# Kernel tuning notes

Measured on AMD Instinct MI355X. Metric: run time of the kernel, lower is better.

## Reference

```python
import jax, jax.numpy as jnp
import numpy as np

N, E, D_IN, HID, H = 50000, 800000, 128, 64, 2
C = HID  # per-head dim (out_channels)


def _lin_params(key, fan_in, fan_out):
    kw, kb = jax.random.split(key)
    s = 1.0 / np.sqrt(fan_in)
    W = jax.random.uniform(kw, (fan_in, fan_out), jnp.float32, -s, s)
    b = jax.random.uniform(kb, (fan_out,), jnp.float32, -s, s)
    return W, b


def setup_inputs() -> dict:
    key = jax.random.key(0)
    ks = jax.random.split(key, 14)
    x = jax.random.normal(ks[0], (N, D_IN), jnp.float32)
    edge_index = jax.random.randint(ks[1], (2, E), 0, N, jnp.int32)
    inp = {"x": x, "edge_index": edge_index}
    dims = [D_IN, HID, HID]
    i = 2
    for L, d_in in enumerate(dims, start=1):
        for nm, fo in (("q", H * C), ("k", H * C), ("v", H * C), ("s", HID)):
            W, b = _lin_params(ks[i], d_in, fo)
            inp[f"W{L}{nm}"] = W
            inp[f"b{L}{nm}"] = b
            i += 1
            if i >= 14:
                ks = jax.random.split(ks[-1], 14)
                i = 0
    return inp


def _transformer_conv(x, src, dst, Wq, bq, Wk, bk, Wv, bv, Ws, bs):
    # x: [N, d_in] -> out: [N, HID]
    q = (x @ Wq + bq).reshape(N, H, C)
    k = (x @ Wk + bk).reshape(N, H, C)
    v = (x @ Wv + bv).reshape(N, H, C)
    qi = q[dst]                      # [E, H, C] gather at destination (query)
    kj = k[src]                      # [E, H, C] gather at source (key)
    alpha = jnp.sum(qi * kj, axis=-1) / jnp.sqrt(jnp.float32(C))  # [E, H]
    amax = jax.ops.segment_max(alpha, dst, num_segments=N)        # [N, H]
    ex = jnp.exp(alpha - amax[dst])                               # [E, H]
    denom = jax.ops.segment_sum(ex, dst, num_segments=N)          # [N, H]
    attn = ex / (denom[dst] + 1e-16)                              # [E, H]
    msg = v[src] * attn[:, :, None]                               # [E, H, C]
    out = jax.ops.segment_sum(msg, dst, num_segments=N)           # [N, H, C]
    out = out.mean(axis=1)                                        # concat=False: head mean
    return out + x @ Ws + bs                                      # root skip


def reference(x, edge_index,
              W1q, b1q, W1k, b1k, W1v, b1v, W1s, b1s,
              W2q, b2q, W2k, b2k, W2v, b2v, W2s, b2s,
              W3q, b3q, W3k, b3k, W3v, b3v, W3s, b3s):
    src, dst = edge_index[0], edge_index[1]
    h = jax.nn.relu(_transformer_conv(x, src, dst, W1q, b1q, W1k, b1k, W1v, b1v, W1s, b1s))
    h = jax.nn.relu(_transformer_conv(h, src, dst, W2q, b2q, W2k, b2k, W2v, b2v, W2s, b2s))
    h = jax.nn.relu(_transformer_conv(h, src, dst, W3q, b3q, W3k, b3k, W3v, b3v, W3s, b3s))
    return h
```

## Files before the change

### kernel.cpp

```cpp
#include <hip/hip_runtime.h>
#include <cstdint>

typedef _Float16 f16;
typedef __attribute__((ext_vector_type(2))) _Float16 f16x2;
typedef __attribute__((ext_vector_type(8))) _Float16 f16x8;
typedef __attribute__((ext_vector_type(4))) float f32x4;

#if defined(__has_builtin)
# if __has_builtin(__builtin_amdgcn_fdot2)
#  define HAVE_FDOT2 1
# endif
#endif


__global__ void hist_kernel(const int* __restrict__ dst, int* __restrict__ cnt, int E) {
    int e = blockIdx.x * blockDim.x + threadIdx.x;
    if (e < E) atomicAdd(&cnt[dst[e]], 1);
}

__global__ __launch_bounds__(256) void block_scan_kernel(
    const int* __restrict__ cnt, int* __restrict__ rowptr,
    int* __restrict__ partials, int n) {
    __shared__ int lds[256];
    int tid = threadIdx.x;
    int i = blockIdx.x * 256 + tid;
    int v = (i < n) ? cnt[i] : 0;
    lds[tid] = v;
    __syncthreads();
    for (int off = 1; off < 256; off <<= 1) {
        int t = (tid >= off) ? lds[tid - off] : 0;
        __syncthreads();
        lds[tid] += t;
        __syncthreads();
    }
    if (i < n) rowptr[i + 1] = lds[tid];
    if (tid == 255) partials[blockIdx.x] = lds[255];
}

__global__ __launch_bounds__(256) void partial_scan_kernel(int* __restrict__ partials, int nb) {
    __shared__ int lds[256];
    int tid = threadIdx.x;
    int v = (tid < nb) ? partials[tid] : 0;
    lds[tid] = v;
    __syncthreads();
    for (int off = 1; off < 256; off <<= 1) {
        int t = (tid >= off) ? lds[tid - off] : 0;
        __syncthreads();
        lds[tid] += t;
        __syncthreads();
    }
    if (tid < nb) partials[tid] = lds[tid] - v;
}

__global__ __launch_bounds__(256) void add_offsets_kernel(
    int* __restrict__ rowptr, const int* __restrict__ partials, int n) {
    int i = blockIdx.x * 256 + threadIdx.x;
    if (i < n) rowptr[i + 1] += partials[blockIdx.x];
    if (i == 0) rowptr[0] = 0;
}

__global__ void scatter_kernel(const int* __restrict__ src, const int* __restrict__ dst,
                               const int* __restrict__ rowptr, int* __restrict__ cnt,
                               int* __restrict__ src_sorted, int E) {
    int e = blockIdx.x * blockDim.x + threadIdx.x;
    if (e < E) {
        int d = dst[e];
        int p = rowptr[d] + atomicAdd(&cnt[d], 1);
        src_sorted[p] = src[e];
    }
}


__global__ __launch_bounds__(256) void prep_w_kernel(
    const float* __restrict__ Wq, const float* __restrict__ Wk,
    const float* __restrict__ Wv, const float* __restrict__ Ws,
    const float* __restrict__ bq, const float* __restrict__ bk,
    const float* __restrict__ bv, const float* __restrict__ bs,
    f16* __restrict__ Wf, float* __restrict__ bias, int K) {
    int idx = blockIdx.x * 256 + threadIdx.x;
    if (idx < 448) {
        bias[idx] = (idx < 128) ? bq[idx]
                  : (idx < 256) ? bk[idx - 128]
                  : (idx < 384) ? bv[idx - 256]
                  : bs[idx - 384];
    }
    if (idx >= 448 * K) return;
    int c = idx / K, k = idx - c * K;
    float v;
    if (c < 128)      v = Wq[k * 128 + c];
    else if (c < 256) v = Wk[k * 128 + (c - 128)];
    else if (c < 384) v = Wv[k * 128 + (c - 256)];
    else              v = Ws[k * 64 + (c - 384)];
    int NK = K >> 5;
    int ct = c >> 6, cf = (c >> 4) & 3, fr = c & 15;
    int ks = k >> 5, fk = (k >> 3) & 3, j = k & 7;
    size_t off = ((size_t)(((ct * 4 + cf) * NK + ks) * 4 + fk) * 16 + fr) * 8 + j;
    Wf[off] = (f16)v;
}


template <int K, bool F32IN>
__global__ __launch_bounds__(256) void gemm_qkvs_kernel(
    const void* __restrict__ Xv, const f16* __restrict__ Wf,
    const float* __restrict__ bias, f16* __restrict__ out, int M) {
    constexpr int NK = K / 32;
    int tid = threadIdx.x;
    int lane = tid & 63, wid = tid >> 6;
    int fr = lane & 15, fk = lane >> 4;
    int arow = blockIdx.x * 64 + wid * 16 + fr;
    int crow = (arow < M) ? arow : (M - 1);

    f16x8 af[NK];
    if (F32IN) {
        const float* X = (const float*)Xv + (size_t)crow * K;
        #pragma unroll
        for (int ks = 0; ks < NK; ++ks) {
            float4 lo = *(const float4*)(X + ks * 32 + fk * 8);
            float4 hi = *(const float4*)(X + ks * 32 + fk * 8 + 4);
            af[ks] = {(f16)lo.x, (f16)lo.y, (f16)lo.z, (f16)lo.w,
                      (f16)hi.x, (f16)hi.y, (f16)hi.z, (f16)hi.w};
        }
    } else {
        const f16* X = (const f16*)Xv + (size_t)crow * K;
        #pragma unroll
        for (int ks = 0; ks < NK; ++ks)
            af[ks] = *(const f16x8*)(X + ks * 32 + fk * 8);
    }

    int orow0 = blockIdx.x * 64 + wid * 16 + fk * 4;
    for (int ct = 0; ct < 7; ++ct) {
        f32x4 acc[4] = {};
        #pragma unroll
        for (int cf = 0; cf < 4; ++cf) {
            const f16* Wp = Wf + (size_t)(ct * 4 + cf) * NK * 512 + (size_t)lane * 8;
            #pragma unroll
            for (int ks = 0; ks < NK; ++ks) {
                f16x8 bf = *(const f16x8*)(Wp + (size_t)ks * 512);
                acc[cf] = __builtin_amdgcn_mfma_f32_16x16x32_f16(af[ks], bf, acc[cf], 0, 0, 0);
            }
        }
        int ocol = ct * 64 + fr;
        #pragma unroll
        for (int cf = 0; cf < 4; ++cf) {
            float b = bias[ocol + cf * 16];
            #pragma unroll
            for (int r = 0; r < 4; ++r) {
                int gr = orow0 + r;
                if (gr < M) out[(size_t)gr * 448 + ocol + cf * 16] = (f16)(acc[cf][r] + b);
            }
        }
    }
}


__global__ __launch_bounds__(256) void attn_kernel(
    const f16* __restrict__ T,
    const int* __restrict__ rowptr, const int* __restrict__ srcs,
    f16* __restrict__ hout, float* __restrict__ fout, int n, int final_layer) {
    int node = blockIdx.x * 4 + (threadIdx.x >> 6);
    if (node >= n) return;
    int lane = threadIdx.x & 63;
    int c8 = lane & 7, eg = lane >> 3;
    const size_t base = (size_t)node * 448;
    const int co = c8 * 8;

    f16x8 q0 = *(const f16x8*)(T + base + co);
    f16x8 q1 = *(const f16x8*)(T + base + 64 + co);
    float m0 = -__builtin_inff(), m1 = -__builtin_inff();
    float s0 = 0.f, s1 = 0.f;
    float av0[8] = {}, av1[8] = {};

    int beg = rowptr[node], end = rowptr[node + 1];
    if (beg < end) {
        int nsrc = srcs[min(beg + eg, end - 1)];
        for (int i0 = beg; i0 < end; i0 += 8) {
            int i = i0 + eg;
            bool valid = (i < end);
            int sidx = nsrc;
            if (i0 + 8 < end) nsrc = srcs[min(i + 8, end - 1)];

            const f16* p = T + (size_t)sidx * 448 + co;
            f16x8 k0 = *(const f16x8*)(p + 128);
            f16x8 k1 = *(const f16x8*)(p + 192);
            f16x8 v0 = *(const f16x8*)(p + 256);
            f16x8 v1 = *(const f16x8*)(p + 320);

            float d0 = 0.f, d1 = 0.f;
#ifdef HAVE_FDOT2
            #pragma unroll
            for (int j = 0; j < 4; ++j) {
                f16x2 a0 = {q0[2 * j], q0[2 * j + 1]};
                f16x2 b0 = {k0[2 * j], k0[2 * j + 1]};
                d0 = __builtin_amdgcn_fdot2(a0, b0, d0, false);
                f16x2 a1 = {q1[2 * j], q1[2 * j + 1]};
                f16x2 b1 = {k1[2 * j], k1[2 * j + 1]};
                d1 = __builtin_amdgcn_fdot2(a1, b1, d1, false);
            }
#else
            #pragma unroll
            for (int j = 0; j < 8; ++j) {
                d0 += (float)q0[j] * (float)k0[j];
                d1 += (float)q1[j] * (float)k1[j];
            }
#endif
            d0 += __shfl_xor(d0, 1); d1 += __shfl_xor(d1, 1);
            d0 += __shfl_xor(d0, 2); d1 += __shfl_xor(d1, 2);
            d0 += __shfl_xor(d0, 4); d1 += __shfl_xor(d1, 4);
            d0 *= 0.125f; d1 *= 0.125f;
            if (!valid) { d0 = -__builtin_inff(); d1 = -__builtin_inff(); }

            if (__any(d0 > m0 + 6.f || d1 > m1 + 6.f)) {
                float t0 = d0, t1 = d1;
                t0 = fmaxf(t0, __shfl_xor(t0, 8));  t1 = fmaxf(t1, __shfl_xor(t1, 8));
                t0 = fmaxf(t0, __shfl_xor(t0, 16)); t1 = fmaxf(t1, __shfl_xor(t1, 16));
                t0 = fmaxf(t0, __shfl_xor(t0, 32)); t1 = fmaxf(t1, __shfl_xor(t1, 32));
                float nm0 = fmaxf(m0, t0), nm1 = fmaxf(m1, t1);
                float f0 = __expf(m0 - nm0), f1 = __expf(m1 - nm1);
                s0 *= f0; s1 *= f1;
                #pragma unroll
                for (int j = 0; j < 8; ++j) { av0[j] *= f0; av1[j] *= f1; }
                m0 = nm0; m1 = nm1;
            }
            float p0 = __expf(d0 - m0);
            float p1 = __expf(d1 - m1);
            s0 += p0; s1 += p1;
            #pragma unroll
            for (int j = 0; j < 8; ++j) {
                av0[j] += p0 * (float)v0[j];
                av1[j] += p1 * (float)v1[j];
            }
        }
    }

    s0 += __shfl_xor(s0, 8);  s1 += __shfl_xor(s1, 8);
    s0 += __shfl_xor(s0, 16); s1 += __shfl_xor(s1, 16);
    s0 += __shfl_xor(s0, 32); s1 += __shfl_xor(s1, 32);
    float inv0 = 1.0f / (s0 + 1e-16f), inv1 = 1.0f / (s1 + 1e-16f);
    float r[8];
    #pragma unroll
    for (int j = 0; j < 8; ++j) {
        float a0 = av0[j], a1 = av1[j];
        a0 += __shfl_xor(a0, 8);  a1 += __shfl_xor(a1, 8);
        a0 += __shfl_xor(a0, 16); a1 += __shfl_xor(a1, 16);
        a0 += __shfl_xor(a0, 32); a1 += __shfl_xor(a1, 32);
        r[j] = 0.5f * (a0 * inv0 + a1 * inv1);
    }

    if (lane < 8) {
        f16x8 sk = *(const f16x8*)(T + base + 384 + co);
        #pragma unroll
        for (int j = 0; j < 8; ++j) r[j] = fmaxf(r[j] + (float)sk[j], 0.f);
        if (final_layer) {
            float4* dst4 = (float4*)(fout + (size_t)node * 64 + co);
            dst4[0] = make_float4(r[0], r[1], r[2], r[3]);
            dst4[1] = make_float4(r[4], r[5], r[6], r[7]);
        } else {
            f16x8 o = {(f16)r[0], (f16)r[1], (f16)r[2], (f16)r[3],
                       (f16)r[4], (f16)r[5], (f16)r[6], (f16)r[7]};
            *(f16x8*)(hout + (size_t)node * 64 + co) = o;
        }
    }
}


extern "C" void kernel_launch(void* const* d_in, const int* in_sizes, int n_in,
                              void* d_out, int out_size, void* d_ws, size_t ws_size,
                              hipStream_t stream) {
    const float* x = (const float*)d_in[0];
    const int* ei  = (const int*)d_in[1];
    const int N = in_sizes[0] / 128;
    const int E = in_sizes[1] / 2;
    const int* src = ei;
    const int* dst = ei + E;

    const float* Wq[3] = {(const float*)d_in[2],  (const float*)d_in[10], (const float*)d_in[18]};
    const float* bq[3] = {(const float*)d_in[3],  (const float*)d_in[11], (const float*)d_in[19]};
    const float* Wk[3] = {(const float*)d_in[4],  (const float*)d_in[12], (const float*)d_in[20]};
    const float* bk[3] = {(const float*)d_in[5],  (const float*)d_in[13], (const float*)d_in[21]};
    const float* Wv[3] = {(const float*)d_in[6],  (const float*)d_in[14], (const float*)d_in[22]};
    const float* bv[3] = {(const float*)d_in[7],  (const float*)d_in[15], (const float*)d_in[23]};
    const float* Wsk[3]= {(const float*)d_in[8],  (const float*)d_in[16], (const float*)d_in[24]};
    const float* bsk[3]= {(const float*)d_in[9],  (const float*)d_in[17], (const float*)d_in[25]};

    char* p = (char*)d_ws;
    int* rowptr   = (int*)p; p += (size_t)(N + 1) * 4;
    int* cnt      = (int*)p; p += (size_t)N * 4;
    int* srcs     = (int*)p; p += (size_t)E * 4;
    int* partials = (int*)p; p += 256 * 4;
    p = (char*)(((uintptr_t)p + 255) & ~(uintptr_t)255);
    f16* Xh   = (f16*)p; p += (size_t)N * 64 * 2;
    f16* QKVS = (f16*)p; p += (size_t)N * 448 * 2;
    f16* Wt0  = (f16*)p; p += (size_t)448 * 128 * 2;
    f16* Wt1  = (f16*)p; p += (size_t)448 * 64 * 2;
    f16* Wt2  = (f16*)p; p += (size_t)448 * 64 * 2;
    float* bias0 = (float*)p; p += 448 * 4;
    float* bias1 = (float*)p; p += 448 * 4;
    float* bias2 = (float*)p; p += 448 * 4;
    if ((size_t)(p - (char*)d_ws) > ws_size) return;

    f16* Wt[3] = {Wt0, Wt1, Wt2};
    float* bias[3] = {bias0, bias1, bias2};

    for (int l = 0; l < 3; ++l) {
        int K = (l == 0) ? 128 : 64;
        prep_w_kernel<<<(448 * K + 255) / 256, 256, 0, stream>>>(
            Wq[l], Wk[l], Wv[l], Wsk[l], bq[l], bk[l], bv[l], bsk[l], Wt[l], bias[l], K);
    }

    int nb = (N + 255) / 256;
    hipMemsetAsync(cnt, 0, (size_t)N * 4, stream);
    hist_kernel<<<(E + 255) / 256, 256, 0, stream>>>(dst, cnt, E);
    block_scan_kernel<<<nb, 256, 0, stream>>>(cnt, rowptr, partials, N);
    partial_scan_kernel<<<1, 256, 0, stream>>>(partials, nb);
    add_offsets_kernel<<<nb, 256, 0, stream>>>(rowptr, partials, N);
    hipMemsetAsync(cnt, 0, (size_t)N * 4, stream);
    scatter_kernel<<<(E + 255) / 256, 256, 0, stream>>>(src, dst, rowptr, cnt, srcs, E);

    int gx = (N + 63) / 64;
    for (int l = 0; l < 3; ++l) {
        if (l == 0)
            gemm_qkvs_kernel<128, true><<<gx, 256, 0, stream>>>(x, Wt[l], bias[l], QKVS, N);
        else
            gemm_qkvs_kernel<64, false><<<gx, 256, 0, stream>>>(Xh, Wt[l], bias[l], QKVS, N);
        attn_kernel<<<(N + 3) / 4, 256, 0, stream>>>(
            QKVS, rowptr, srcs, Xh, (float*)d_out, N, (l == 2) ? 1 : 0);
    }
}
```

Before: 358.6 us.

## Merge weight-prep launches, fold count reset into scan, prefetch K/V, shrink attn blocks

```diff
diff --git a/kernel.cpp b/kernel.cpp
--- a/kernel.cpp
+++ b/kernel.cpp
@@ -19,7 +19,7 @@
 }
 
 __global__ __launch_bounds__(256) void block_scan_kernel(
-    const int* __restrict__ cnt, int* __restrict__ rowptr,
+    int* __restrict__ cnt, int* __restrict__ rowptr,
     int* __restrict__ partials, int n) {
     __shared__ int lds[256];
     int tid = threadIdx.x;
@@ -33,7 +33,7 @@
         lds[tid] += t;
         __syncthreads();
     }
-    if (i < n) rowptr[i + 1] = lds[tid];
+    if (i < n) { rowptr[i + 1] = lds[tid]; cnt[i] = 0; }
     if (tid == 255) partials[blockIdx.x] = lds[255];
 }
 
@@ -71,31 +71,35 @@
 }
 
 
-__global__ __launch_bounds__(256) void prep_w_kernel(
-    const float* __restrict__ Wq, const float* __restrict__ Wk,
-    const float* __restrict__ Wv, const float* __restrict__ Ws,
-    const float* __restrict__ bq, const float* __restrict__ bk,
-    const float* __restrict__ bv, const float* __restrict__ bs,
-    f16* __restrict__ Wf, float* __restrict__ bias, int K) {
+struct PrepArgs {
+    const float* Wq[3]; const float* Wk[3]; const float* Wv[3]; const float* Ws[3];
+    const float* bq[3]; const float* bk[3]; const float* bv[3]; const float* bs[3];
+    f16* Wf[3]; float* bias[3];
+};
+
+__global__ __launch_bounds__(256) void prep_w_all_kernel(PrepArgs a) {
     int idx = blockIdx.x * 256 + threadIdx.x;
-    if (idx < 448) {
-        bias[idx] = (idx < 128) ? bq[idx]
-                  : (idx < 256) ? bk[idx - 128]
-                  : (idx < 384) ? bv[idx - 256]
-                  : bs[idx - 384];
-    }
-    if (idx >= 448 * K) return;
-    int c = idx / K, k = idx - c * K;
+    int l, loc, K;
+    if (idx < 448 * 128)      { l = 0; loc = idx;              K = 128; }
+    else if (idx < 448 * 192) { l = 1; loc = idx - 448 * 128;  K = 64;  }
+    else                      { l = 2; loc = idx - 448 * 192;  K = 64;  }
+    if (loc < 448) {
+        a.bias[l][loc] = (loc < 128) ? a.bq[l][loc]
+                       : (loc < 256) ? a.bk[l][loc - 128]
+                       : (loc < 384) ? a.bv[l][loc - 256]
+                       : a.bs[l][loc - 384];
+    }
+    int c = loc / K, k = loc - c * K;
     float v;
-    if (c < 128)      v = Wq[k * 128 + c];
-    else if (c < 256) v = Wk[k * 128 + (c - 128)];
-    else if (c < 384) v = Wv[k * 128 + (c - 256)];
-    else              v = Ws[k * 64 + (c - 384)];
+    if (c < 128)      v = a.Wq[l][k * 128 + c];
+    else if (c < 256) v = a.Wk[l][k * 128 + (c - 128)];
+    else if (c < 384) v = a.Wv[l][k * 128 + (c - 256)];
+    else              v = a.Ws[l][k * 64 + (c - 384)];
     int NK = K >> 5;
     int ct = c >> 6, cf = (c >> 4) & 3, fr = c & 15;
     int ks = k >> 5, fk = (k >> 3) & 3, j = k & 7;
     size_t off = ((size_t)(((ct * 4 + cf) * NK + ks) * 4 + fk) * 16 + fr) * 8 + j;
-    Wf[off] = (f16)v;
+    a.Wf[l][off] = (f16)v;
 }
 
 
@@ -153,11 +157,11 @@
 }
 
 
-__global__ __launch_bounds__(256) void attn_kernel(
+__global__ __launch_bounds__(128) void attn_kernel(
     const f16* __restrict__ T,
     const int* __restrict__ rowptr, const int* __restrict__ srcs,
     f16* __restrict__ hout, float* __restrict__ fout, int n, int final_layer) {
-    int node = blockIdx.x * 4 + (threadIdx.x >> 6);
+    int node = blockIdx.x * 2 + (threadIdx.x >> 6);
     if (node >= n) return;
     int lane = threadIdx.x & 63;
     int c8 = lane & 7, eg = lane >> 3;
@@ -172,62 +176,78 @@
 
     int beg = rowptr[node], end = rowptr[node + 1];
     if (beg < end) {
-        int nsrc = srcs[min(beg + eg, end - 1)];
-        for (int i0 = beg; i0 < end; i0 += 8) {
-            int i = i0 + eg;
-            bool valid = (i < end);
-            int sidx = nsrc;
-            if (i0 + 8 < end) nsrc = srcs[min(i + 8, end - 1)];
-
-            const f16* p = T + (size_t)sidx * 448 + co;
+        int i = beg + eg;
+        bool valid = (i < end);
+        {
+            const f16* p = T + (size_t)srcs[valid ? i : (end - 1)] * 448 + co;
             f16x8 k0 = *(const f16x8*)(p + 128);
             f16x8 k1 = *(const f16x8*)(p + 192);
             f16x8 v0 = *(const f16x8*)(p + 256);
             f16x8 v1 = *(const f16x8*)(p + 320);
 
-            float d0 = 0.f, d1 = 0.f;
+            for (int i0 = beg; i0 < end; i0 += 8) {
+                bool have_next = (i0 + 8) < end;
+                bool nvalid = false;
+                f16x8 nk0, nk1, nv0, nv1;
+                if (have_next) {
+                    int ni = i0 + 8 + eg;
+                    nvalid = (ni < end);
+                    const f16* np = T + (size_t)srcs[nvalid ? ni : (end - 1)] * 448 + co;
+                    nk0 = *(const f16x8*)(np + 128);
+                    nk1 = *(const f16x8*)(np + 192);
+                    nv0 = *(const f16x8*)(np + 256);
+                    nv1 = *(const f16x8*)(np + 320);
+                }
+
+                float d0 = 0.f, d1 = 0.f;
 #ifdef HAVE_FDOT2
-            #pragma unroll
-            for (int j = 0; j < 4; ++j) {
-                f16x2 a0 = {q0[2 * j], q0[2 * j + 1]};
-                f16x2 b0 = {k0[2 * j], k0[2 * j + 1]};
-                d0 = __builtin_amdgcn_fdot2(a0, b0, d0, false);
-                f16x2 a1 = {q1[2 * j], q1[2 * j + 1]};
-                f16x2 b1 = {k1[2 * j], k1[2 * j + 1]};
-                d1 = __builtin_amdgcn_fdot2(a1, b1, d1, false);
-            }
+                #pragma unroll
+                for (int j = 0; j < 4; ++j) {
+                    f16x2 a0 = {q0[2 * j], q0[2 * j + 1]};
+                    f16x2 b0 = {k0[2 * j], k0[2 * j + 1]};
+                    d0 = __builtin_amdgcn_fdot2(a0, b0, d0, false);
+                    f16x2 a1 = {q1[2 * j], q1[2 * j + 1]};
+                    f16x2 b1 = {k1[2 * j], k1[2 * j + 1]};
+                    d1 = __builtin_amdgcn_fdot2(a1, b1, d1, false);
+                }
 #else
-            #pragma unroll
-            for (int j = 0; j < 8; ++j) {
-                d0 += (float)q0[j] * (float)k0[j];
-                d1 += (float)q1[j] * (float)k1[j];
-            }
+                #pragma unroll
+                for (int j = 0; j < 8; ++j) {
+                    d0 += (float)q0[j] * (float)k0[j];
+                    d1 += (float)q1[j] * (float)k1[j];
+                }
 #endif
-            d0 += __shfl_xor(d0, 1); d1 += __shfl_xor(d1, 1);
-            d0 += __shfl_xor(d0, 2); d1 += __shfl_xor(d1, 2);
-            d0 += __shfl_xor(d0, 4); d1 += __shfl_xor(d1, 4);
-            d0 *= 0.125f; d1 *= 0.125f;
-            if (!valid) { d0 = -__builtin_inff(); d1 = -__builtin_inff(); }
-
-            if (__any(d0 > m0 + 6.f || d1 > m1 + 6.f)) {
-                float t0 = d0, t1 = d1;
-                t0 = fmaxf(t0, __shfl_xor(t0, 8));  t1 = fmaxf(t1, __shfl_xor(t1, 8));
-                t0 = fmaxf(t0, __shfl_xor(t0, 16)); t1 = fmaxf(t1, __shfl_xor(t1, 16));
-                t0 = fmaxf(t0, __shfl_xor(t0, 32)); t1 = fmaxf(t1, __shfl_xor(t1, 32));
-                float nm0 = fmaxf(m0, t0), nm1 = fmaxf(m1, t1);
-                float f0 = __expf(m0 - nm0), f1 = __expf(m1 - nm1);
-                s0 *= f0; s1 *= f1;
+                d0 += __shfl_xor(d0, 1); d1 += __shfl_xor(d1, 1);
+                d0 += __shfl_xor(d0, 2); d1 += __shfl_xor(d1, 2);
+                d0 += __shfl_xor(d0, 4); d1 += __shfl_xor(d1, 4);
+                d0 *= 0.125f; d1 *= 0.125f;
+                if (!valid) { d0 = -__builtin_inff(); d1 = -__builtin_inff(); }
+
+                if (__any(d0 > m0 + 6.f || d1 > m1 + 6.f)) {
+                    float t0 = d0, t1 = d1;
+                    t0 = fmaxf(t0, __shfl_xor(t0, 8));  t1 = fmaxf(t1, __shfl_xor(t1, 8));
+                    t0 = fmaxf(t0, __shfl_xor(t0, 16)); t1 = fmaxf(t1, __shfl_xor(t1, 16));
+                    t0 = fmaxf(t0, __shfl_xor(t0, 32)); t1 = fmaxf(t1, __shfl_xor(t1, 32));
+                    float nm0 = fmaxf(m0, t0), nm1 = fmaxf(m1, t1);
+                    float f0 = __expf(m0 - nm0), f1 = __expf(m1 - nm1);
+                    s0 *= f0; s1 *= f1;
+                    #pragma unroll
+                    for (int j = 0; j < 8; ++j) { av0[j] *= f0; av1[j] *= f1; }
+                    m0 = nm0; m1 = nm1;
+                }
+                float p0 = __expf(d0 - m0);
+                float p1 = __expf(d1 - m1);
+                s0 += p0; s1 += p1;
                 #pragma unroll
-                for (int j = 0; j < 8; ++j) { av0[j] *= f0; av1[j] *= f1; }
-                m0 = nm0; m1 = nm1;
-            }
-            float p0 = __expf(d0 - m0);
-            float p1 = __expf(d1 - m1);
-            s0 += p0; s1 += p1;
-            #pragma unroll
-            for (int j = 0; j < 8; ++j) {
-                av0[j] += p0 * (float)v0[j];
-                av1[j] += p1 * (float)v1[j];
+                for (int j = 0; j < 8; ++j) {
+                    av0[j] += p0 * (float)v0[j];
+                    av1[j] += p1 * (float)v1[j];
+                }
+
+                if (have_next) {
+                    k0 = nk0; k1 = nk1; v0 = nv0; v1 = nv1;
+                    valid = nvalid;
+                }
             }
         }
     }
@@ -272,15 +292,6 @@
     const int E = in_sizes[1] / 2;
     const int* src = ei;
     const int* dst = ei + E;
-
-    const float* Wq[3] = {(const float*)d_in[2],  (const float*)d_in[10], (const float*)d_in[18]};
-    const float* bq[3] = {(const float*)d_in[3],  (const float*)d_in[11], (const float*)d_in[19]};
-    const float* Wk[3] = {(const float*)d_in[4],  (const float*)d_in[12], (const float*)d_in[20]};
-    const float* bk[3] = {(const float*)d_in[5],  (const float*)d_in[13], (const float*)d_in[21]};
-    const float* Wv[3] = {(const float*)d_in[6],  (const float*)d_in[14], (const float*)d_in[22]};
-    const float* bv[3] = {(const float*)d_in[7],  (const float*)d_in[15], (const float*)d_in[23]};
-    const float* Wsk[3]= {(const float*)d_in[8],  (const float*)d_in[16], (const float*)d_in[24]};
-    const float* bsk[3]= {(const float*)d_in[9],  (const float*)d_in[17], (const float*)d_in[25]};
 
     char* p = (char*)d_ws;
     int* rowptr   = (int*)p; p += (size_t)(N + 1) * 4;
@@ -298,31 +309,39 @@
     float* bias2 = (float*)p; p += 448 * 4;
     if ((size_t)(p - (char*)d_ws) > ws_size) return;
 
-    f16* Wt[3] = {Wt0, Wt1, Wt2};
-    float* bias[3] = {bias0, bias1, bias2};
-
+    PrepArgs pa;
     for (int l = 0; l < 3; ++l) {
-        int K = (l == 0) ? 128 : 64;
-        prep_w_kernel<<<(448 * K + 255) / 256, 256, 0, stream>>>(
-            Wq[l], Wk[l], Wv[l], Wsk[l], bq[l], bk[l], bv[l], bsk[l], Wt[l], bias[l], K);
-    }
+        pa.Wq[l] = (const float*)d_in[2 + 8 * l];
+        pa.bq[l] = (const float*)d_in[3 + 8 * l];
+        pa.Wk[l] = (const float*)d_in[4 + 8 * l];
+        pa.bk[l] = (const float*)d_in[5 + 8 * l];
+        pa.Wv[l] = (const float*)d_in[6 + 8 * l];
+        pa.bv[l] = (const float*)d_in[7 + 8 * l];
+        pa.Ws[l] = (const float*)d_in[8 + 8 * l];
+        pa.bs[l] = (const float*)d_in[9 + 8 * l];
+    }
+    pa.Wf[0] = Wt0; pa.Wf[1] = Wt1; pa.Wf[2] = Wt2;
+    pa.bias[0] = bias0; pa.bias[1] = bias1; pa.bias[2] = bias2;
+
+    hipMemsetAsync(cnt, 0, (size_t)N * 4, stream);
+    prep_w_all_kernel<<<448, 256, 0, stream>>>(pa);
 
     int nb = (N + 255) / 256;
-    hipMemsetAsync(cnt, 0, (size_t)N * 4, stream);
     hist_kernel<<<(E + 255) / 256, 256, 0, stream>>>(dst, cnt, E);
     block_scan_kernel<<<nb, 256, 0, stream>>>(cnt, rowptr, partials, N);
     partial_scan_kernel<<<1, 256, 0, stream>>>(partials, nb);
     add_offsets_kernel<<<nb, 256, 0, stream>>>(rowptr, partials, N);
-    hipMemsetAsync(cnt, 0, (size_t)N * 4, stream);
     scatter_kernel<<<(E + 255) / 256, 256, 0, stream>>>(src, dst, rowptr, cnt, srcs, E);
 
     int gx = (N + 63) / 64;
+    f16* Wt[3] = {Wt0, Wt1, Wt2};
+    float* bias[3] = {bias0, bias1, bias2};
     for (int l = 0; l < 3; ++l) {
         if (l == 0)
             gemm_qkvs_kernel<128, true><<<gx, 256, 0, stream>>>(x, Wt[l], bias[l], QKVS, N);
         else
             gemm_qkvs_kernel<64, false><<<gx, 256, 0, stream>>>(Xh, Wt[l], bias[l], QKVS, N);
-        attn_kernel<<<(N + 3) / 4, 256, 0, stream>>>(
+        attn_kernel<<<(N + 1) / 2, 128, 0, stream>>>(
             QKVS, rowptr, srcs, Xh, (float*)d_out, N, (l == 2) ? 1 : 0);
     }
 }
```

Measured after the change: 363.6 us. About the same (+1.4%).
